# Kernel tuning notes

Hardware: AMD Instinct MI355X
Metric: run time of the kernel (lower is better)

The kernel has to match this reference:

```python
import jax, jax.numpy as jnp
import numpy as np

N_NODES = 50000
N_EDGES = 800000
HIDDEN = 128
NUM_GDL = 2


def setup_inputs() -> dict:
    key = jax.random.key(0)
    k0, k1, k2, k3, k4 = jax.random.split(key, 5)
    x = jax.random.normal(k0, (N_NODES, HIDDEN), dtype=jnp.float32)
    row = jax.random.randint(k1, (N_EDGES,), 0, N_NODES, dtype=jnp.int32)
    # ensure every node appears at least once as a target so degree >= 1
    col_tail = jax.random.randint(k2, (N_EDGES - N_NODES,), 0, N_NODES, dtype=jnp.int32)
    col = jnp.concatenate([jnp.arange(N_NODES, dtype=jnp.int32), col_tail])
    edge_index = jnp.stack([row, col], axis=0)  # [2, E]
    W1s = jax.random.normal(k3, (NUM_GDL, HIDDEN, HIDDEN), dtype=jnp.float32) / np.sqrt(HIDDEN).astype(np.float32)
    W2s = jax.random.normal(k4, (NUM_GDL, HIDDEN, 2 * HIDDEN), dtype=jnp.float32) / np.sqrt(2 * HIDDEN).astype(np.float32)
    biases = jnp.zeros((NUM_GDL, HIDDEN), dtype=jnp.float32)  # reset_parameters zeroes bias
    return {"x": x, "edge_index": edge_index, "W1s": W1s, "W2s": W2s, "biases": biases}


def reference(x, edge_index, W1s, W2s, biases):
    # eval mode: dropout is identity
    row, col = edge_index[0], edge_index[1]  # row = source j, col = target i
    n, d = x.shape
    deg = jax.ops.segment_sum(jnp.ones(row.shape[0], x.dtype), col, num_segments=n)
    norm = (1.0 / deg)[row]  # per-edge norm, indexed by row as in torch source
    for k in range(W1s.shape[0]):
        W1, W2, b = W1s[k], W2s[k], biases[k]
        # lin2(cat[x_i, x_j]) = x_i @ W2[:, :d].T + x_j @ W2[:, d:].T
        # precompute both node-level projections, then gather per edge (cheaper than per-edge GEMM)
        proj_i = x @ W2[:, :d].T  # [n, d]
        proj_j = x @ W2[:, d:].T  # [n, d]
        msg = norm[:, None] * (proj_i[col] + proj_j[row])  # [E, d]
        agg = jax.ops.segment_sum(msg, col, num_segments=n)  # scatter-add into targets
        out = x @ W1.T - agg + b
        x = jax.nn.gelu(out, approximate=False)  # torch nn.GELU default = exact erf
    return x
```

## Files before the change

### kernel.cpp

```cpp
#include <hip/hip_runtime.h>

#define N_NODES 50000
#define N_EDGES 800000
#define D 128
#define NBUCKET 196
#define EPT 16
#define HIST_BLOCKS 196
#define WCONV_BLOCKS 96
#define CAST_BLOCKS 6250
#define GEMM_TILES 391

typedef unsigned short ushort_t;
typedef __bf16 bf16x8 __attribute__((ext_vector_type(8)));
typedef float f32x4 __attribute__((ext_vector_type(4)));

__device__ __forceinline__ ushort_t f2bf(float f) {
    unsigned u = __builtin_bit_cast(unsigned, f);
    u += 0x7FFFu + ((u >> 16) & 1u);
    return (ushort_t)(u >> 16);
}
__device__ __forceinline__ float bf2f(unsigned h16) {
    return __builtin_bit_cast(float, h16 << 16);
}

__global__ __launch_bounds__(256) void k_pre(const float* __restrict__ x, ushort_t* __restrict__ xb,
                                             const int* __restrict__ col, int* __restrict__ bucket_cnt,
                                             const float* __restrict__ W1s, const float* __restrict__ W2s,
                                             ushort_t* __restrict__ Wb) {
    __shared__ int hist[NBUCKET];
    int b = blockIdx.x;
    if (b < HIST_BLOCKS) {
        for (int t = threadIdx.x; t < NBUCKET; t += 256) hist[t] = 0;
        __syncthreads();
        int base = (b * 256 + threadIdx.x) * EPT;
        if (base < N_EDGES) {
            int4 c[4];
            #pragma unroll
            for (int q = 0; q < 4; ++q) c[q] = *(const int4*)(col + base + q * 4);
            #pragma unroll
            for (int q = 0; q < 4; ++q) {
                atomicAdd(&hist[c[q].x >> 8], 1); atomicAdd(&hist[c[q].y >> 8], 1);
                atomicAdd(&hist[c[q].z >> 8], 1); atomicAdd(&hist[c[q].w >> 8], 1);
            }
        }
        __syncthreads();
        for (int t = threadIdx.x; t < NBUCKET; t += 256) {
            int v = hist[t];
            if (v) atomicAdd(&bucket_cnt[t], v);
        }
    } else if (b < HIST_BLOCKS + WCONV_BLOCKS) {
        int c = (b - HIST_BLOCKS) * 256 + threadIdx.x;
        int k = c / 12288, rem = c % 12288;
        int mat = rem / 4096, rr = (rem % 4096) / 32, col4 = rem % 32;
        const float* src = (mat == 0)
            ? (W1s + k * 16384 + rr * 128 + col4 * 4)
            : (W2s + k * 32768 + rr * 256 + (mat == 2 ? 128 : 0) + col4 * 4);
        float4 v = *(const float4*)src;
        ushort_t tmp[4] = { f2bf(v.x), f2bf(v.y), f2bf(v.z), f2bf(v.w) };
        *(uint2*)(Wb + ((size_t)(k * 3 + mat)) * 16384 + rr * 128 + col4 * 4) = *(const uint2*)tmp;
    } else {
        int base = ((b - HIST_BLOCKS - WCONV_BLOCKS) * 256 + threadIdx.x) * 4;
        if (base < N_NODES * D) {
            float4 v = *(const float4*)(x + base);
            ushort_t tmp[4] = { f2bf(v.x), f2bf(v.y), f2bf(v.z), f2bf(v.w) };
            *(uint2*)(xb + base) = *(const uint2*)tmp;
        }
    }
}

__global__ __launch_bounds__(256) void k_bscan(const int* __restrict__ bucket_cnt,
                                               int* __restrict__ bucket_base,
                                               int* __restrict__ bucket_cursor) {
    __shared__ int sm[256];
    int t = threadIdx.x;
    int v = (t < NBUCKET) ? bucket_cnt[t] : 0;
    sm[t] = v;
    __syncthreads();
    for (int o = 1; o < 256; o <<= 1) {
        int add = (t >= o) ? sm[t - o] : 0;
        __syncthreads();
        sm[t] += add;
        __syncthreads();
    }
    if (t < NBUCKET) {
        int excl = sm[t] - v;
        bucket_base[t] = excl;
        bucket_cursor[t] = excl;
    }
}

__device__ __forceinline__ void gemm_tile(int m0, int y,
                                          ushort_t (*As)[136], ushort_t (*Bs)[136],
                                          const ushort_t* __restrict__ xb,
                                          const ushort_t* __restrict__ Wl,
                                          ushort_t* __restrict__ Plb,
                                          ushort_t* __restrict__ Pi_,
                                          ushort_t* __restrict__ Pj) {
    const ushort_t* Wmat = Wl + (size_t)y * 16384;
    const int tid = threadIdx.x;

    #pragma unroll
    for (int it = 0; it < 8; ++it) {
        int c = tid + it * 256;
        int r = c >> 4, kc = c & 15;
        uint4 v = make_uint4(0, 0, 0, 0);
        int gm = m0 + r;
        if (gm < N_NODES) v = *(const uint4*)(xb + (size_t)gm * D + kc * 8);
        *(uint4*)&As[r][kc * 8] = v;
    }
    #pragma unroll
    for (int it = 0; it < 8; ++it) {
        int c = tid + it * 256;
        int r = c >> 4, kc = c & 15;
        *(uint4*)&Bs[r][kc * 8] = *(const uint4*)(Wmat + r * 128 + kc * 8);
    }
    __syncthreads();

    const int w = tid >> 6, lane = tid & 63, quad = lane >> 4, r16 = lane & 15;
    f32x4 acc[2][8];
    #pragma unroll
    for (int mt = 0; mt < 2; ++mt)
        #pragma unroll
        for (int nt = 0; nt < 8; ++nt) acc[mt][nt] = (f32x4){0.f, 0.f, 0.f, 0.f};
    const int arow0 = w * 32 + r16, arow1 = arow0 + 16;
    #pragma unroll
    for (int k0 = 0; k0 < 128; k0 += 32) {
        bf16x8 a0 = __builtin_bit_cast(bf16x8, *(const uint4*)&As[arow0][k0 + quad * 8]);
        bf16x8 a1 = __builtin_bit_cast(bf16x8, *(const uint4*)&As[arow1][k0 + quad * 8]);
        #pragma unroll
        for (int nt = 0; nt < 8; ++nt) {
            bf16x8 b = __builtin_bit_cast(bf16x8, *(const uint4*)&Bs[nt * 16 + r16][k0 + quad * 8]);
            acc[0][nt] = __builtin_amdgcn_mfma_f32_16x16x32_bf16(b, a0, acc[0][nt], 0, 0, 0);
            acc[1][nt] = __builtin_amdgcn_mfma_f32_16x16x32_bf16(b, a1, acc[1][nt], 0, 0, 0);
        }
    }
    ushort_t* Outp = (y == 0) ? Plb : (y == 1 ? Pi_ : Pj);
    #pragma unroll
    for (int mt = 0; mt < 2; ++mt) {
        int gm = m0 + w * 32 + mt * 16 + r16;
        if (gm >= N_NODES) continue;
        #pragma unroll
        for (int nt = 0; nt < 8; ++nt) {
            ushort_t tmp[4] = { f2bf(acc[mt][nt][0]), f2bf(acc[mt][nt][1]),
                                f2bf(acc[mt][nt][2]), f2bf(acc[mt][nt][3]) };
            *(uint2*)(Outp + (size_t)gm * D + nt * 16 + quad * 4) = *(const uint2*)tmp;
        }
    }
}

__global__ __launch_bounds__(256) void k_scatter_gemm(const int* __restrict__ row, const int* __restrict__ col,
                                                      int* __restrict__ bucket_cursor, int2* __restrict__ temp,
                                                      const ushort_t* __restrict__ xb,
                                                      const ushort_t* __restrict__ Wb,
                                                      ushort_t* __restrict__ Plb,
                                                      ushort_t* __restrict__ Pi_,
                                                      ushort_t* __restrict__ Pj) {
    __shared__ __align__(16) ushort_t As[128][136];
    __shared__ __align__(16) ushort_t Bs[128][136];
    __shared__ int hist[NBUCKET];
    if (blockIdx.x < HIST_BLOCKS) {
        for (int t = threadIdx.x; t < NBUCKET; t += 256) hist[t] = 0;
        __syncthreads();
        int base = (blockIdx.x * 256 + threadIdx.x) * EPT;
        bool act = base < N_EDGES;
        int4 c[4], r[4];
        if (act) {
            #pragma unroll
            for (int q = 0; q < 4; ++q) c[q] = *(const int4*)(col + base + q * 4);
            #pragma unroll
            for (int q = 0; q < 4; ++q) r[q] = *(const int4*)(row + base + q * 4);
            #pragma unroll
            for (int q = 0; q < 4; ++q) {
                atomicAdd(&hist[c[q].x >> 8], 1); atomicAdd(&hist[c[q].y >> 8], 1);
                atomicAdd(&hist[c[q].z >> 8], 1); atomicAdd(&hist[c[q].w >> 8], 1);
            }
        }
        __syncthreads();
        for (int t = threadIdx.x; t < NBUCKET; t += 256) {
            int cnt = hist[t];
            hist[t] = cnt ? atomicAdd(&bucket_cursor[t], cnt) : 0;
        }
        __syncthreads();
        if (act) {
            #pragma unroll
            for (int q = 0; q < 4; ++q) {
                int cc[4] = { c[q].x, c[q].y, c[q].z, c[q].w };
                int rr[4] = { r[q].x, r[q].y, r[q].z, r[q].w };
                #pragma unroll
                for (int e = 0; e < 4; ++e) {
                    int pos = atomicAdd(&hist[cc[e] >> 8], 1);
                    temp[pos] = make_int2(rr[e], cc[e]);
                }
            }
        }
    } else {
        int g = blockIdx.x - HIST_BLOCKS;
        int y = g % 3, tile = g / 3;
        gemm_tile(tile * 128, y, As, Bs, xb, Wb, Plb, Pi_, Pj);
    }
}

__global__ __launch_bounds__(256) void k_bsort(const int2* __restrict__ temp,
                                               const int* __restrict__ bucket_base,
                                               const int* __restrict__ bucket_cnt,
                                               int* __restrict__ csr, int* __restrict__ off,
                                               int* __restrict__ deg, float* __restrict__ inv_deg) {
    __shared__ int hist[256];
    __shared__ int sm[256];
    int b = blockIdx.x, t = threadIdx.x;
    int base = bucket_base[b], cnt = bucket_cnt[b];
    hist[t] = 0;
    __syncthreads();
    int i = t;
    for (; i + 768 < cnt; i += 1024) {
        int2 e0 = temp[base + i], e1 = temp[base + i + 256];
        int2 e2 = temp[base + i + 512], e3 = temp[base + i + 768];
        atomicAdd(&hist[e0.y & 255], 1); atomicAdd(&hist[e1.y & 255], 1);
        atomicAdd(&hist[e2.y & 255], 1); atomicAdd(&hist[e3.y & 255], 1);
    }
    for (; i < cnt; i += 256) {
        int2 e = temp[base + i];
        atomicAdd(&hist[e.y & 255], 1);
    }
    __syncthreads();
    int c = hist[t];
    sm[t] = c;
    __syncthreads();
    for (int o = 1; o < 256; o <<= 1) {
        int add = (t >= o) ? sm[t - o] : 0;
        __syncthreads();
        sm[t] += add;
        __syncthreads();
    }
    int excl = sm[t] - c;
    int node = b * 256 + t;
    if (node < N_NODES) {
        off[node] = base + excl;
        deg[node] = c;
        inv_deg[node] = 1.0f / (float)c;
    }
    __syncthreads();
    hist[t] = base + excl;
    __syncthreads();
    i = t;
    for (; i + 768 < cnt; i += 1024) {
        int2 e0 = temp[base + i], e1 = temp[base + i + 256];
        int2 e2 = temp[base + i + 512], e3 = temp[base + i + 768];
        int p0 = atomicAdd(&hist[e0.y & 255], 1);
        int p1 = atomicAdd(&hist[e1.y & 255], 1);
        int p2 = atomicAdd(&hist[e2.y & 255], 1);
        int p3 = atomicAdd(&hist[e3.y & 255], 1);
        csr[p0] = e0.x; csr[p1] = e1.x; csr[p2] = e2.x; csr[p3] = e3.x;
    }
    for (; i < cnt; i += 256) {
        int2 e = temp[base + i];
        int p = atomicAdd(&hist[e.y & 255], 1);
        csr[p] = e.x;
    }
}

__global__ __launch_bounds__(256) void k_gemm(const ushort_t* __restrict__ xb,
                                              const ushort_t* __restrict__ Wl,
                                              ushort_t* __restrict__ Plb,
                                              ushort_t* __restrict__ Pi_,
                                              ushort_t* __restrict__ Pj) {
    __shared__ __align__(16) ushort_t As[128][136];
    __shared__ __align__(16) ushort_t Bs[128][136];
    gemm_tile(blockIdx.x * 128, blockIdx.y, As, Bs, xb, Wl, Plb, Pi_, Pj);
}

__global__ __launch_bounds__(256) void k_agg(const ushort_t* __restrict__ Plb,
                                             const ushort_t* __restrict__ Pi_,
                                             const ushort_t* __restrict__ Pj,
                                             const int* __restrict__ off,
                                             const int* __restrict__ deg,
                                             const int* __restrict__ csr,
                                             const float* __restrict__ inv_deg,
                                             const float* __restrict__ bias,
                                             float* __restrict__ out_f32,
                                             ushort_t* __restrict__ out_bf16,
                                             int write_bf16) {
    int wv = __builtin_amdgcn_readfirstlane(threadIdx.x >> 6);
    int node = blockIdx.x * 4 + wv;
    int lane = threadIdx.x & 63;
    if (node >= N_NODES) return;
    unsigned ulin = *(const unsigned*)(Plb + (size_t)node * D + 2 * lane);
    unsigned upi  = *(const unsigned*)(Pi_ + (size_t)node * D + 2 * lane);
    float2 bv = *(const float2*)(bias + 2 * lane);
    float a0 = bf2f(ulin & 0xffffu) + bv.x;
    float a1 = bf2f(ulin >> 16)     + bv.y;
    float c0 = 0.f, c1 = 0.f, si = 0.f, sj = 0.f;
    int e0 = off[node], ne = deg[node];
    int j = 0;
    for (; j + 16 <= ne; j += 16) {
        int sx[16];
        #pragma unroll
        for (int t = 0; t < 16; ++t) sx[t] = csr[e0 + j + t];
        unsigned p[16];
        #pragma unroll
        for (int t = 0; t < 16; ++t) p[t] = *(const unsigned*)(Pj + (size_t)sx[t] * D + 2 * lane);
        float dv[16];
        #pragma unroll
        for (int t = 0; t < 16; ++t) dv[t] = inv_deg[sx[t]];
        #pragma unroll
        for (int t = 0; t < 16; t += 2) {
            si += dv[t];
            sj += dv[t + 1];
            a0 -= dv[t] * bf2f(p[t] & 0xffffu) + dv[t + 1] * bf2f(p[t + 1] & 0xffffu);
            a1 -= dv[t] * bf2f(p[t] >> 16)     + dv[t + 1] * bf2f(p[t + 1] >> 16);
        }
    }
    for (; j + 4 <= ne; j += 4) {
        int s0 = csr[e0 + j], s1 = csr[e0 + j + 1], s2 = csr[e0 + j + 2], s3 = csr[e0 + j + 3];
        unsigned p0 = *(const unsigned*)(Pj + (size_t)s0 * D + 2 * lane);
        unsigned p1 = *(const unsigned*)(Pj + (size_t)s1 * D + 2 * lane);
        unsigned p2 = *(const unsigned*)(Pj + (size_t)s2 * D + 2 * lane);
        unsigned p3 = *(const unsigned*)(Pj + (size_t)s3 * D + 2 * lane);
        float d0 = inv_deg[s0], d1 = inv_deg[s1], d2 = inv_deg[s2], d3 = inv_deg[s3];
        si += d0 + d2; sj += d1 + d3;
        a0 -= d0 * bf2f(p0 & 0xffffu) + d1 * bf2f(p1 & 0xffffu);
        a1 -= d0 * bf2f(p0 >> 16)     + d1 * bf2f(p1 >> 16);
        c0 += d2 * bf2f(p2 & 0xffffu) + d3 * bf2f(p3 & 0xffffu);
        c1 += d2 * bf2f(p2 >> 16)     + d3 * bf2f(p3 >> 16);
    }
    for (; j < ne; ++j) {
        int s0 = csr[e0 + j];
        unsigned p0 = *(const unsigned*)(Pj + (size_t)s0 * D + 2 * lane);
        float d0 = inv_deg[s0];
        si += d0;
        a0 -= d0 * bf2f(p0 & 0xffffu);
        a1 -= d0 * bf2f(p0 >> 16);
    }
    si += sj;
    a0 -= c0 + si * bf2f(upi & 0xffffu);
    a1 -= c1 + si * bf2f(upi >> 16);
    float g0 = 0.5f * a0 * (1.0f + erff(a0 * 0.70710678118654752440f));
    float g1 = 0.5f * a1 * (1.0f + erff(a1 * 0.70710678118654752440f));
    if (write_bf16) {
        ushort_t tmp[2] = { f2bf(g0), f2bf(g1) };
        *(unsigned*)(out_bf16 + (size_t)node * D + 2 * lane) = *(const unsigned*)tmp;
    } else {
        *(float2*)(out_f32 + (size_t)node * D + 2 * lane) = make_float2(g0, g1);
    }
}

extern "C" void kernel_launch(void* const* d_in, const int* in_sizes, int n_in,
                              void* d_out, int out_size, void* d_ws, size_t ws_size,
                              hipStream_t stream) {
    const float* x      = (const float*)d_in[0];
    const int*   ei     = (const int*)d_in[1];
    const int*   rowp   = ei;
    const int*   colp   = ei + N_EDGES;
    const float* W1s    = (const float*)d_in[2];
    const float* W2s    = (const float*)d_in[3];
    const float* biases = (const float*)d_in[4];
    float* out = (float*)d_out;

    char* ws = (char*)d_ws;
    size_t o = 0;
    auto carve = [&](size_t bytes) -> void* {
        void* p = ws + o;
        o = (o + bytes + 255) & ~(size_t)255;
        return p;
    };
    int*      bucket_cnt    = (int*)carve(NBUCKET * 4);
    int*      bucket_base   = (int*)carve(NBUCKET * 4);
    int*      bucket_cursor = (int*)carve(NBUCKET * 4);
    int*      deg     = (int*)carve(N_NODES * 4);
    float*    inv_deg = (float*)carve(N_NODES * 4);
    int*      off     = (int*)carve(N_NODES * 4);
    int*      csr     = (int*)carve(N_EDGES * 4);
    int2*     temp    = (int2*)carve((size_t)N_EDGES * 8);
    ushort_t* xb      = (ushort_t*)carve((size_t)N_NODES * D * 2);
    ushort_t* Wb      = (ushort_t*)carve((size_t)2 * 3 * 16384 * 2);
    ushort_t* Plb     = (ushort_t*)carve((size_t)N_NODES * D * 2);
    ushort_t* Pi_     = (ushort_t*)carve((size_t)N_NODES * D * 2);
    ushort_t* Pj      = (ushort_t*)carve((size_t)N_NODES * D * 2);
    if (o > ws_size) return;

    hipMemsetAsync(bucket_cnt, 0, NBUCKET * 4, stream);

    k_pre<<<HIST_BLOCKS + WCONV_BLOCKS + CAST_BLOCKS, 256, 0, stream>>>(x, xb, colp, bucket_cnt,
                                                                        W1s, W2s, Wb);
    k_bscan<<<1, 256, 0, stream>>>(bucket_cnt, bucket_base, bucket_cursor);
    k_scatter_gemm<<<HIST_BLOCKS + 3 * GEMM_TILES, 256, 0, stream>>>(rowp, colp, bucket_cursor, temp,
                                                                     xb, Wb, Plb, Pi_, Pj);
    k_bsort<<<NBUCKET, 256, 0, stream>>>(temp, bucket_base, bucket_cnt, csr, off, deg, inv_deg);

    const int AB = (N_NODES + 3) / 4;
    k_agg<<<AB, 256, 0, stream>>>(Plb, Pi_, Pj, off, deg, csr, inv_deg, biases,
                                  nullptr, xb, 1);
    k_gemm<<<dim3(GEMM_TILES, 3), 256, 0, stream>>>(xb, Wb + (size_t)3 * 16384, Plb, Pi_, Pj);
    k_agg<<<AB, 256, 0, stream>>>(Plb, Pi_, Pj, off, deg, csr, inv_deg, biases + 128,
                                  out, nullptr, 0);
}
```

Measured before the change: 226.0 us.

## Scatter edges into fixed-capacity buckets, drop bucket scan, fuse sort with 3-way GEMM

Edges are now scattered into fixed-capacity per-bucket slots (CAP 8192) during the preprocessing kernel, so the separate histogram pass, the single-block bucket scan and one launch are no longer needed. Each bucket-sort block derives its global base with an in-block prefix over bucket counts. The bucket sort now runs in the same launch as the projection GEMM. Each GEMM block computes all three weight projections, reusing its A tile, which cuts the block count threefold. The fixed capacity risks overflow if any bucket exceeds 8192 edges (the expected count is about 4096) and enlarges the temp buffer. Each GEMM block also becomes longer and more serial.

```diff
diff --git a/kernel.cpp b/kernel.cpp
--- a/kernel.cpp
+++ b/kernel.cpp
@@ -4,8 +4,9 @@
 #define N_EDGES 800000
 #define D 128
 #define NBUCKET 196
+#define CAP 8192
 #define EPT 16
-#define HIST_BLOCKS 196
+#define SCAT_BLOCKS 196
 #define WCONV_BLOCKS 96
 #define CAST_BLOCKS 6250
 #define GEMM_TILES 391
@@ -24,19 +25,23 @@
 }
 
 __global__ __launch_bounds__(256) void k_pre(const float* __restrict__ x, ushort_t* __restrict__ xb,
-                                             const int* __restrict__ col, int* __restrict__ bucket_cnt,
+                                             const int* __restrict__ row, const int* __restrict__ col,
+                                             int* __restrict__ bucket_cursor, int2* __restrict__ temp,
                                              const float* __restrict__ W1s, const float* __restrict__ W2s,
                                              ushort_t* __restrict__ Wb) {
     __shared__ int hist[NBUCKET];
     int b = blockIdx.x;
-    if (b < HIST_BLOCKS) {
+    if (b < SCAT_BLOCKS) {
         for (int t = threadIdx.x; t < NBUCKET; t += 256) hist[t] = 0;
         __syncthreads();
         int base = (b * 256 + threadIdx.x) * EPT;
-        if (base < N_EDGES) {
-            int4 c[4];
+        bool act = base < N_EDGES;
+        int4 c[4], r[4];
+        if (act) {
             #pragma unroll
             for (int q = 0; q < 4; ++q) c[q] = *(const int4*)(col + base + q * 4);
+            #pragma unroll
+            for (int q = 0; q < 4; ++q) r[q] = *(const int4*)(row + base + q * 4);
             #pragma unroll
             for (int q = 0; q < 4; ++q) {
                 atomicAdd(&hist[c[q].x >> 8], 1); atomicAdd(&hist[c[q].y >> 8], 1);
@@ -45,11 +50,25 @@
         }
         __syncthreads();
         for (int t = threadIdx.x; t < NBUCKET; t += 256) {
-            int v = hist[t];
-            if (v) atomicAdd(&bucket_cnt[t], v);
-        }
-    } else if (b < HIST_BLOCKS + WCONV_BLOCKS) {
-        int c = (b - HIST_BLOCKS) * 256 + threadIdx.x;
+            int cnt = hist[t];
+            hist[t] = cnt ? atomicAdd(&bucket_cursor[t], cnt) : 0;
+        }
+        __syncthreads();
+        if (act) {
+            #pragma unroll
+            for (int q = 0; q < 4; ++q) {
+                int cc[4] = { c[q].x, c[q].y, c[q].z, c[q].w };
+                int rr[4] = { r[q].x, r[q].y, r[q].z, r[q].w };
+                #pragma unroll
+                for (int e = 0; e < 4; ++e) {
+                    int bk = cc[e] >> 8;
+                    int pos = atomicAdd(&hist[bk], 1);
+                    temp[bk * CAP + pos] = make_int2(rr[e], cc[e]);
+                }
+            }
+        }
+    } else if (b < SCAT_BLOCKS + WCONV_BLOCKS) {
+        int c = (b - SCAT_BLOCKS) * 256 + threadIdx.x;
         int k = c / 12288, rem = c % 12288;
         int mat = rem / 4096, rr = (rem % 4096) / 32, col4 = rem % 32;
         const float* src = (mat == 0)
@@ -59,7 +78,7 @@
         ushort_t tmp[4] = { f2bf(v.x), f2bf(v.y), f2bf(v.z), f2bf(v.w) };
         *(uint2*)(Wb + ((size_t)(k * 3 + mat)) * 16384 + rr * 128 + col4 * 4) = *(const uint2*)tmp;
     } else {
-        int base = ((b - HIST_BLOCKS - WCONV_BLOCKS) * 256 + threadIdx.x) * 4;
+        int base = ((b - SCAT_BLOCKS - WCONV_BLOCKS) * 256 + threadIdx.x) * 4;
         if (base < N_NODES * D) {
             float4 v = *(const float4*)(x + base);
             ushort_t tmp[4] = { f2bf(v.x), f2bf(v.y), f2bf(v.z), f2bf(v.w) };
@@ -68,37 +87,14 @@
     }
 }
 
-__global__ __launch_bounds__(256) void k_bscan(const int* __restrict__ bucket_cnt,
-                                               int* __restrict__ bucket_base,
-                                               int* __restrict__ bucket_cursor) {
-    __shared__ int sm[256];
-    int t = threadIdx.x;
-    int v = (t < NBUCKET) ? bucket_cnt[t] : 0;
-    sm[t] = v;
-    __syncthreads();
-    for (int o = 1; o < 256; o <<= 1) {
-        int add = (t >= o) ? sm[t - o] : 0;
-        __syncthreads();
-        sm[t] += add;
-        __syncthreads();
-    }
-    if (t < NBUCKET) {
-        int excl = sm[t] - v;
-        bucket_base[t] = excl;
-        bucket_cursor[t] = excl;
-    }
-}
-
-__device__ __forceinline__ void gemm_tile(int m0, int y,
-                                          ushort_t (*As)[136], ushort_t (*Bs)[136],
-                                          const ushort_t* __restrict__ xb,
-                                          const ushort_t* __restrict__ Wl,
-                                          ushort_t* __restrict__ Plb,
-                                          ushort_t* __restrict__ Pi_,
-                                          ushort_t* __restrict__ Pj) {
-    const ushort_t* Wmat = Wl + (size_t)y * 16384;
+__device__ __forceinline__ void gemm_tile3(int m0,
+                                           ushort_t (*As)[136], ushort_t (*Bs)[136],
+                                           const ushort_t* __restrict__ xb,
+                                           const ushort_t* __restrict__ Wl,
+                                           ushort_t* __restrict__ Plb,
+                                           ushort_t* __restrict__ Pi_,
+                                           ushort_t* __restrict__ Pj) {
     const int tid = threadIdx.x;
-
     #pragma unroll
     for (int it = 0; it < 8; ++it) {
         int c = tid + it * 256;
@@ -108,154 +104,123 @@
         if (gm < N_NODES) v = *(const uint4*)(xb + (size_t)gm * D + kc * 8);
         *(uint4*)&As[r][kc * 8] = v;
     }
-    #pragma unroll
-    for (int it = 0; it < 8; ++it) {
-        int c = tid + it * 256;
-        int r = c >> 4, kc = c & 15;
-        *(uint4*)&Bs[r][kc * 8] = *(const uint4*)(Wmat + r * 128 + kc * 8);
-    }
-    __syncthreads();
-
     const int w = tid >> 6, lane = tid & 63, quad = lane >> 4, r16 = lane & 15;
-    f32x4 acc[2][8];
-    #pragma unroll
-    for (int mt = 0; mt < 2; ++mt)
-        #pragma unroll
-        for (int nt = 0; nt < 8; ++nt) acc[mt][nt] = (f32x4){0.f, 0.f, 0.f, 0.f};
     const int arow0 = w * 32 + r16, arow1 = arow0 + 16;
     #pragma unroll
-    for (int k0 = 0; k0 < 128; k0 += 32) {
-        bf16x8 a0 = __builtin_bit_cast(bf16x8, *(const uint4*)&As[arow0][k0 + quad * 8]);
-        bf16x8 a1 = __builtin_bit_cast(bf16x8, *(const uint4*)&As[arow1][k0 + quad * 8]);
-        #pragma unroll
-        for (int nt = 0; nt < 8; ++nt) {
-            bf16x8 b = __builtin_bit_cast(bf16x8, *(const uint4*)&Bs[nt * 16 + r16][k0 + quad * 8]);
-            acc[0][nt] = __builtin_amdgcn_mfma_f32_16x16x32_bf16(b, a0, acc[0][nt], 0, 0, 0);
-            acc[1][nt] = __builtin_amdgcn_mfma_f32_16x16x32_bf16(b, a1, acc[1][nt], 0, 0, 0);
-        }
-    }
-    ushort_t* Outp = (y == 0) ? Plb : (y == 1 ? Pi_ : Pj);
-    #pragma unroll
-    for (int mt = 0; mt < 2; ++mt) {
-        int gm = m0 + w * 32 + mt * 16 + r16;
-        if (gm >= N_NODES) continue;
-        #pragma unroll
-        for (int nt = 0; nt < 8; ++nt) {
-            ushort_t tmp[4] = { f2bf(acc[mt][nt][0]), f2bf(acc[mt][nt][1]),
-                                f2bf(acc[mt][nt][2]), f2bf(acc[mt][nt][3]) };
-            *(uint2*)(Outp + (size_t)gm * D + nt * 16 + quad * 4) = *(const uint2*)tmp;
-        }
-    }
-}
-
-__global__ __launch_bounds__(256) void k_scatter_gemm(const int* __restrict__ row, const int* __restrict__ col,
-                                                      int* __restrict__ bucket_cursor, int2* __restrict__ temp,
-                                                      const ushort_t* __restrict__ xb,
-                                                      const ushort_t* __restrict__ Wb,
-                                                      ushort_t* __restrict__ Plb,
-                                                      ushort_t* __restrict__ Pi_,
-                                                      ushort_t* __restrict__ Pj) {
+    for (int y = 0; y < 3; ++y) {
+        const ushort_t* Wmat = Wl + (size_t)y * 16384;
+        #pragma unroll
+        for (int it = 0; it < 8; ++it) {
+            int c = tid + it * 256;
+            int r = c >> 4, kc = c & 15;
+            *(uint4*)&Bs[r][kc * 8] = *(const uint4*)(Wmat + r * 128 + kc * 8);
+        }
+        __syncthreads();
+        f32x4 acc[2][8];
+        #pragma unroll
+        for (int mt = 0; mt < 2; ++mt)
+            #pragma unroll
+            for (int nt = 0; nt < 8; ++nt) acc[mt][nt] = (f32x4){0.f, 0.f, 0.f, 0.f};
+        #pragma unroll
+        for (int k0 = 0; k0 < 128; k0 += 32) {
+            bf16x8 a0 = __builtin_bit_cast(bf16x8, *(const uint4*)&As[arow0][k0 + quad * 8]);
+            bf16x8 a1 = __builtin_bit_cast(bf16x8, *(const uint4*)&As[arow1][k0 + quad * 8]);
+            #pragma unroll
+            for (int nt = 0; nt < 8; ++nt) {
+                bf16x8 b = __builtin_bit_cast(bf16x8, *(const uint4*)&Bs[nt * 16 + r16][k0 + quad * 8]);
+                acc[0][nt] = __builtin_amdgcn_mfma_f32_16x16x32_bf16(b, a0, acc[0][nt], 0, 0, 0);
+                acc[1][nt] = __builtin_amdgcn_mfma_f32_16x16x32_bf16(b, a1, acc[1][nt], 0, 0, 0);
+            }
+        }
+        ushort_t* Outp = (y == 0) ? Plb : (y == 1 ? Pi_ : Pj);
+        #pragma unroll
+        for (int mt = 0; mt < 2; ++mt) {
+            int gm = m0 + w * 32 + mt * 16 + r16;
+            if (gm >= N_NODES) continue;
+            #pragma unroll
+            for (int nt = 0; nt < 8; ++nt) {
+                ushort_t tmp[4] = { f2bf(acc[mt][nt][0]), f2bf(acc[mt][nt][1]),
+                                    f2bf(acc[mt][nt][2]), f2bf(acc[mt][nt][3]) };
+                *(uint2*)(Outp + (size_t)gm * D + nt * 16 + quad * 4) = *(const uint2*)tmp;
+            }
+        }
+        if (y < 2) __syncthreads();
+    }
+}
+
+__global__ __launch_bounds__(256) void k_bsort_gemm(const int2* __restrict__ temp,
+                                                    const int* __restrict__ bucket_cursor,
+                                                    int* __restrict__ csr, int* __restrict__ off,
+                                                    int* __restrict__ deg, float* __restrict__ inv_deg,
+                                                    const ushort_t* __restrict__ xb,
+                                                    const ushort_t* __restrict__ Wb,
+                                                    ushort_t* __restrict__ Plb,
+                                                    ushort_t* __restrict__ Pi_,
+                                                    ushort_t* __restrict__ Pj) {
     __shared__ __align__(16) ushort_t As[128][136];
     __shared__ __align__(16) ushort_t Bs[128][136];
-    __shared__ int hist[NBUCKET];
-    if (blockIdx.x < HIST_BLOCKS) {
-        for (int t = threadIdx.x; t < NBUCKET; t += 256) hist[t] = 0;
-        __syncthreads();
-        int base = (blockIdx.x * 256 + threadIdx.x) * EPT;
-        bool act = base < N_EDGES;
-        int4 c[4], r[4];
-        if (act) {
-            #pragma unroll
-            for (int q = 0; q < 4; ++q) c[q] = *(const int4*)(col + base + q * 4);
-            #pragma unroll
-            for (int q = 0; q < 4; ++q) r[q] = *(const int4*)(row + base + q * 4);
-            #pragma unroll
-            for (int q = 0; q < 4; ++q) {
-                atomicAdd(&hist[c[q].x >> 8], 1); atomicAdd(&hist[c[q].y >> 8], 1);
-                atomicAdd(&hist[c[q].z >> 8], 1); atomicAdd(&hist[c[q].w >> 8], 1);
-            }
-        }
-        __syncthreads();
-        for (int t = threadIdx.x; t < NBUCKET; t += 256) {
-            int cnt = hist[t];
-            hist[t] = cnt ? atomicAdd(&bucket_cursor[t], cnt) : 0;
-        }
-        __syncthreads();
-        if (act) {
-            #pragma unroll
-            for (int q = 0; q < 4; ++q) {
-                int cc[4] = { c[q].x, c[q].y, c[q].z, c[q].w };
-                int rr[4] = { r[q].x, r[q].y, r[q].z, r[q].w };
-                #pragma unroll
-                for (int e = 0; e < 4; ++e) {
-                    int pos = atomicAdd(&hist[cc[e] >> 8], 1);
-                    temp[pos] = make_int2(rr[e], cc[e]);
-                }
-            }
-        }
-    } else {
-        int g = blockIdx.x - HIST_BLOCKS;
-        int y = g % 3, tile = g / 3;
-        gemm_tile(tile * 128, y, As, Bs, xb, Wb, Plb, Pi_, Pj);
-    }
-}
-
-__global__ __launch_bounds__(256) void k_bsort(const int2* __restrict__ temp,
-                                               const int* __restrict__ bucket_base,
-                                               const int* __restrict__ bucket_cnt,
-                                               int* __restrict__ csr, int* __restrict__ off,
-                                               int* __restrict__ deg, float* __restrict__ inv_deg) {
     __shared__ int hist[256];
     __shared__ int sm[256];
-    int b = blockIdx.x, t = threadIdx.x;
-    int base = bucket_base[b], cnt = bucket_cnt[b];
-    hist[t] = 0;
-    __syncthreads();
-    int i = t;
-    for (; i + 768 < cnt; i += 1024) {
-        int2 e0 = temp[base + i], e1 = temp[base + i + 256];
-        int2 e2 = temp[base + i + 512], e3 = temp[base + i + 768];
-        atomicAdd(&hist[e0.y & 255], 1); atomicAdd(&hist[e1.y & 255], 1);
-        atomicAdd(&hist[e2.y & 255], 1); atomicAdd(&hist[e3.y & 255], 1);
-    }
-    for (; i < cnt; i += 256) {
-        int2 e = temp[base + i];
-        atomicAdd(&hist[e.y & 255], 1);
-    }
-    __syncthreads();
-    int c = hist[t];
-    sm[t] = c;
-    __syncthreads();
-    for (int o = 1; o < 256; o <<= 1) {
-        int add = (t >= o) ? sm[t - o] : 0;
-        __syncthreads();
-        sm[t] += add;
-        __syncthreads();
-    }
-    int excl = sm[t] - c;
-    int node = b * 256 + t;
-    if (node < N_NODES) {
-        off[node] = base + excl;
-        deg[node] = c;
-        inv_deg[node] = 1.0f / (float)c;
-    }
-    __syncthreads();
-    hist[t] = base + excl;
-    __syncthreads();
-    i = t;
-    for (; i + 768 < cnt; i += 1024) {
-        int2 e0 = temp[base + i], e1 = temp[base + i + 256];
-        int2 e2 = temp[base + i + 512], e3 = temp[base + i + 768];
-        int p0 = atomicAdd(&hist[e0.y & 255], 1);
-        int p1 = atomicAdd(&hist[e1.y & 255], 1);
-        int p2 = atomicAdd(&hist[e2.y & 255], 1);
-        int p3 = atomicAdd(&hist[e3.y & 255], 1);
-        csr[p0] = e0.x; csr[p1] = e1.x; csr[p2] = e2.x; csr[p3] = e3.x;
-    }
-    for (; i < cnt; i += 256) {
-        int2 e = temp[base + i];
-        int p = atomicAdd(&hist[e.y & 255], 1);
-        csr[p] = e.x;
+    if (blockIdx.x < NBUCKET) {
+        int b = blockIdx.x, t = threadIdx.x;
+        int cnt = bucket_cursor[b];
+        sm[t] = (t < b) ? bucket_cursor[t] : 0;
+        __syncthreads();
+        for (int o = 1; o < 256; o <<= 1) {
+            int add = (t >= o) ? sm[t - o] : 0;
+            __syncthreads();
+            sm[t] += add;
+            __syncthreads();
+        }
+        int gbase = sm[255];
+        int tbase = b * CAP;
+        hist[t] = 0;
+        __syncthreads();
+        int i = t;
+        for (; i + 768 < cnt; i += 1024) {
+            int2 e0 = temp[tbase + i], e1 = temp[tbase + i + 256];
+            int2 e2 = temp[tbase + i + 512], e3 = temp[tbase + i + 768];
+            atomicAdd(&hist[e0.y & 255], 1); atomicAdd(&hist[e1.y & 255], 1);
+            atomicAdd(&hist[e2.y & 255], 1); atomicAdd(&hist[e3.y & 255], 1);
+        }
+        for (; i < cnt; i += 256) atomicAdd(&hist[temp[tbase + i].y & 255], 1);
+        __syncthreads();
+        int c = hist[t];
+        sm[t] = c;
+        __syncthreads();
+        for (int o = 1; o < 256; o <<= 1) {
+            int add = (t >= o) ? sm[t - o] : 0;
+            __syncthreads();
+            sm[t] += add;
+            __syncthreads();
+        }
+        int excl = sm[t] - c;
+        int node = b * 256 + t;
+        if (node < N_NODES) {
+            off[node] = gbase + excl;
+            deg[node] = c;
+            inv_deg[node] = 1.0f / (float)c;
+        }
+        __syncthreads();
+        hist[t] = gbase + excl;
+        __syncthreads();
+        i = t;
+        for (; i + 768 < cnt; i += 1024) {
+            int2 e0 = temp[tbase + i], e1 = temp[tbase + i + 256];
+            int2 e2 = temp[tbase + i + 512], e3 = temp[tbase + i + 768];
+            int p0 = atomicAdd(&hist[e0.y & 255], 1);
+            int p1 = atomicAdd(&hist[e1.y & 255], 1);
+            int p2 = atomicAdd(&hist[e2.y & 255], 1);
+            int p3 = atomicAdd(&hist[e3.y & 255], 1);
+            csr[p0] = e0.x; csr[p1] = e1.x; csr[p2] = e2.x; csr[p3] = e3.x;
+        }
+        for (; i < cnt; i += 256) {
+            int2 e = temp[tbase + i];
+            int p = atomicAdd(&hist[e.y & 255], 1);
+            csr[p] = e.x;
+        }
+    } else {
+        gemm_tile3((blockIdx.x - NBUCKET) * 128, As, Bs, xb, Wb, Plb, Pi_, Pj);
     }
 }
 
@@ -266,7 +231,7 @@
                                               ushort_t* __restrict__ Pj) {
     __shared__ __align__(16) ushort_t As[128][136];
     __shared__ __align__(16) ushort_t Bs[128][136];
-    gemm_tile(blockIdx.x * 128, blockIdx.y, As, Bs, xb, Wl, Plb, Pi_, Pj);
+    gemm_tile3(blockIdx.x * 128, As, Bs, xb, Wl, Plb, Pi_, Pj);
 }
 
 __global__ __launch_bounds__(256) void k_agg(const ushort_t* __restrict__ Plb,
@@ -363,14 +328,12 @@
         o = (o + bytes + 255) & ~(size_t)255;
         return p;
     };
-    int*      bucket_cnt    = (int*)carve(NBUCKET * 4);
-    int*      bucket_base   = (int*)carve(NBUCKET * 4);
     int*      bucket_cursor = (int*)carve(NBUCKET * 4);
     int*      deg     = (int*)carve(N_NODES * 4);
     float*    inv_deg = (float*)carve(N_NODES * 4);
     int*      off     = (int*)carve(N_NODES * 4);
     int*      csr     = (int*)carve(N_EDGES * 4);
-    int2*     temp    = (int2*)carve((size_t)N_EDGES * 8);
+    int2*     temp    = (int2*)carve((size_t)NBUCKET * CAP * 8);
     ushort_t* xb      = (ushort_t*)carve((size_t)N_NODES * D * 2);
     ushort_t* Wb      = (ushort_t*)carve((size_t)2 * 3 * 16384 * 2);
     ushort_t* Plb     = (ushort_t*)carve((size_t)N_NODES * D * 2);
@@ -378,19 +341,18 @@
     ushort_t* Pj      = (ushort_t*)carve((size_t)N_NODES * D * 2);
     if (o > ws_size) return;
 
-    hipMemsetAsync(bucket_cnt, 0, NBUCKET * 4, stream);
-
-    k_pre<<<HIST_BLOCKS + WCONV_BLOCKS + CAST_BLOCKS, 256, 0, stream>>>(x, xb, colp, bucket_cnt,
+    hipMemsetAsync(bucket_cursor, 0, NBUCKET * 4, stream);
+
+    k_pre<<<SCAT_BLOCKS + WCONV_BLOCKS + CAST_BLOCKS, 256, 0, stream>>>(x, xb, rowp, colp,
+                                                                        bucket_cursor, temp,
                                                                         W1s, W2s, Wb);
-    k_bscan<<<1, 256, 0, stream>>>(bucket_cnt, bucket_base, bucket_cursor);
-    k_scatter_gemm<<<HIST_BLOCKS + 3 * GEMM_TILES, 256, 0, stream>>>(rowp, colp, bucket_cursor, temp,
-                                                                     xb, Wb, Plb, Pi_, Pj);
-    k_bsort<<<NBUCKET, 256, 0, stream>>>(temp, bucket_base, bucket_cnt, csr, off, deg, inv_deg);
+    k_bsort_gemm<<<NBUCKET + GEMM_TILES, 256, 0, stream>>>(temp, bucket_cursor, csr, off,
+                                                           deg, inv_deg, xb, Wb, Plb, Pi_, Pj);
 
     const int AB = (N_NODES + 3) / 4;
     k_agg<<<AB, 256, 0, stream>>>(Plb, Pi_, Pj, off, deg, csr, inv_deg, biases,
                                   nullptr, xb, 1);
-    k_gemm<<<dim3(GEMM_TILES, 3), 256, 0, stream>>>(xb, Wb + (size_t)3 * 16384, Plb, Pi_, Pj);
+    k_gemm<<<GEMM_TILES, 256, 0, stream>>>(xb, Wb + (size_t)3 * 16384, Plb, Pi_, Pj);
     k_agg<<<AB, 256, 0, stream>>>(Plb, Pi_, Pj, off, deg, csr, inv_deg, biases + 128,
                                   out, nullptr, 0);
 }
```

Result: faster. 216.9 us (-4.0%).
